# Kernel tuning notes

Hardware: AMD Instinct MI355X
Metric: run time of the kernel (lower is better)

The kernel has to match this reference:

```python
import jax, jax.numpy as jnp
import numpy as np

N, M, D = 2048, 2048, 8


def setup_inputs() -> dict:
    key = jax.random.key(0)
    k1, k2 = jax.random.split(key)
    x = jax.random.normal(k1, (N, D), dtype=jnp.float32)
    xx = jax.random.normal(k2, (M, D), dtype=jnp.float32)
    # free-form params: positive(p) = exp(p); free_form(1.0) = log(1.0) = 0
    scale_free = jnp.zeros((D,), dtype=jnp.float32)
    variance_free = jnp.zeros((), dtype=jnp.float32)
    return {"x": x, "xx": xx, "scale_free": scale_free, "variance_free": variance_free}


def reference(x, xx, scale_free, variance_free):
    # RBF.matrices(x, xx, d_dx=True, d_dxx=True, d_dxdxx=True)
    iscale = 1.0 / jnp.exp(scale_free)            # [D]
    variance = jnp.exp(variance_free)             # scalar, = self.diag()
    r = (x[:, None, :] - xx[None, :, :]) * iscale  # [N,M,D]
    cov = jnp.exp(-0.5 * jnp.sum(r * r, axis=-1)) * variance  # [N,M]
    rr = r * iscale                                # [N,M,D]
    cov_r = cov[..., None] * rr                    # [N,M,D]
    dx = -cov_r                                    # dK/dx
    dxx = cov_r                                    # dK/dxx
    # rirj[..., i, j] = -rr_i * rr_j ; add iscale^2 on the diagonal
    rirj = -rr[..., :, None] * rr[..., None, :] + jnp.diag(iscale * iscale)  # [N,M,D,D]
    dxdxx = rirj * cov[..., None, None]            # d2K/dx dxx
    return (cov, dx, dxx, dxdxx)
```

## Files before the change

kernel.cpp:

```cpp
#include <hip/hip_runtime.h>

#define PN 2048
#define PM 2048
#define PD 8


#define NM_TOT   (PN * PM)
#define BLOCKS_A (NM_TOT * 16 / 256)
#define BLOCKS_B (NM_TOT * 2 / 256)
#define BLOCKS_C (NM_TOT / 256)

__global__ void rbf_precompute(const float* __restrict__ scale_free,
                               const float* __restrict__ var_free,
                               float* __restrict__ ws) {
    const int t = threadIdx.x;
    if (t < PD) {
        const float is = __expf(-scale_free[t]);
        ws[t]     = is;
        ws[9 + t] = is * is;
    }
    if (t == PD) ws[8] = __expf(var_free[0]);
}

__global__ __launch_bounds__(256) void rbf_all_kernel(
    const float* __restrict__ x,
    const float* __restrict__ xx,
    const float* __restrict__ ws,
    float* __restrict__ out)
{
    const unsigned tid = threadIdx.x;
    const unsigned bid = blockIdx.x;

    float is[PD], is2[PD];
#pragma unroll
    for (int d = 0; d < PD; ++d) { is[d] = ws[d]; is2[d] = ws[9 + d]; }
    const float variance = ws[8];

    const size_t NM = (size_t)PN * PM;
    float* covp   = out;
    float* dxp    = out + NM;
    float* dxxp   = out + NM + NM * PD;
    float* dxdxxp = out + NM + 2 * NM * PD;

    auto compute_pair = [&](unsigned p, float r[PD]) -> float {
        const unsigned n = p >> 11;
        const unsigned m = p & 2047u;
        const float4* x4  = reinterpret_cast<const float4*>(x  + (size_t)n * PD);
        const float4* xx4 = reinterpret_cast<const float4*>(xx + (size_t)m * PD);
        const float4 xa = x4[0],  xb = x4[1];
        const float4 ya = xx4[0], yb = xx4[1];
        r[0] = (xa.x - ya.x) * is[0];
        r[1] = (xa.y - ya.y) * is[1];
        r[2] = (xa.z - ya.z) * is[2];
        r[3] = (xa.w - ya.w) * is[3];
        r[4] = (xb.x - yb.x) * is[4];
        r[5] = (xb.y - yb.y) * is[5];
        r[6] = (xb.z - yb.z) * is[6];
        r[7] = (xb.w - yb.w) * is[7];
        float s = 0.f;
#pragma unroll
        for (int d = 0; d < PD; ++d) s += r[d] * r[d];
        return __expf(-0.5f * s) * variance;
    };

    if (bid < BLOCKS_A) {
        const unsigned g = bid * 256u + tid;
        const unsigned p = g >> 4;
        const unsigned i = g & 15u;
        float r[PD];
        const float cov = compute_pair(p, r);
        float rr[PD];
#pragma unroll
        for (int d = 0; d < PD; ++d) rr[d] = r[d] * is[d];

        const unsigned row = i >> 1;
        const unsigned c0  = (i & 1u) * 4u;
        const float a = -cov * rr[row];
        float v[4];
#pragma unroll
        for (int j = 0; j < 4; ++j) v[j] = a * rr[c0 + j];
        if (row >= c0 && row < c0 + 4u) v[row - c0] += cov * is2[row];

        float4* d2 = reinterpret_cast<float4*>(dxdxxp + (size_t)g * 4);
        *d2 = make_float4(v[0], v[1], v[2], v[3]);
    } else if (bid < BLOCKS_A + BLOCKS_B) {
        const unsigned g = (bid - BLOCKS_A) * 256u + tid;
        const unsigned p = g >> 1;
        const unsigned c0 = (g & 1u) * 4u;
        float r[PD];
        const float cov = compute_pair(p, r);
        float w[4];
#pragma unroll
        for (int j = 0; j < 4; ++j) w[j] = cov * r[c0 + j] * is[c0 + j];

        float4* ddx  = reinterpret_cast<float4*>(dxp  + (size_t)g * 4);
        float4* ddxx = reinterpret_cast<float4*>(dxxp + (size_t)g * 4);
        *ddx  = make_float4(-w[0], -w[1], -w[2], -w[3]);
        *ddxx = make_float4( w[0],  w[1],  w[2],  w[3]);
    } else {
        const unsigned p = (bid - BLOCKS_A - BLOCKS_B) * 256u + tid;
        float r[PD];
        covp[p] = compute_pair(p, r);
    }
}

extern "C" void kernel_launch(void* const* d_in, const int* in_sizes, int n_in,
                              void* d_out, int out_size, void* d_ws, size_t ws_size,
                              hipStream_t stream) {
    const float* x  = (const float*)d_in[0];
    const float* xx = (const float*)d_in[1];
    const float* sf = (const float*)d_in[2];
    const float* vf = (const float*)d_in[3];
    float* out = (float*)d_out;
    float* ws  = (float*)d_ws;

    rbf_precompute<<<1, 64, 0, stream>>>(sf, vf, ws);

    const int grid = BLOCKS_A + BLOCKS_B + BLOCKS_C;
    rbf_all_kernel<<<grid, 256, 0, stream>>>(x, xx, ws, out);
}
```

Measured before the change: 1.423 ms.

## Compute each pair once per thread and share via LDS for all outputs

```diff
diff --git a/kernel.cpp b/kernel.cpp
--- a/kernel.cpp
+++ b/kernel.cpp
@@ -4,11 +4,8 @@
 #define PM 2048
 #define PD 8
 
+#define NM ((size_t)PN * (size_t)PM)
 
-#define NM_TOT   (PN * PM)
-#define BLOCKS_A (NM_TOT * 16 / 256)
-#define BLOCKS_B (NM_TOT * 2 / 256)
-#define BLOCKS_C (NM_TOT / 256)
 
 __global__ void rbf_precompute(const float* __restrict__ scale_free,
                                const float* __restrict__ var_free,
@@ -28,79 +25,93 @@
     const float* __restrict__ ws,
     float* __restrict__ out)
 {
+    __shared__ __align__(16) float lds[256 * 12];
+
     const unsigned tid = threadIdx.x;
     const unsigned bid = blockIdx.x;
 
-    float is[PD], is2[PD];
+    float is[PD];
 #pragma unroll
-    for (int d = 0; d < PD; ++d) { is[d] = ws[d]; is2[d] = ws[9 + d]; }
+    for (int d = 0; d < PD; ++d) is[d] = ws[d];
     const float variance = ws[8];
 
-    const size_t NM = (size_t)PN * PM;
     float* covp   = out;
     float* dxp    = out + NM;
     float* dxxp   = out + NM + NM * PD;
     float* dxdxxp = out + NM + 2 * NM * PD;
 
-    auto compute_pair = [&](unsigned p, float r[PD]) -> float {
-        const unsigned n = p >> 11;
-        const unsigned m = p & 2047u;
-        const float4* x4  = reinterpret_cast<const float4*>(x  + (size_t)n * PD);
-        const float4* xx4 = reinterpret_cast<const float4*>(xx + (size_t)m * PD);
-        const float4 xa = x4[0],  xb = x4[1];
-        const float4 ya = xx4[0], yb = xx4[1];
-        r[0] = (xa.x - ya.x) * is[0];
-        r[1] = (xa.y - ya.y) * is[1];
-        r[2] = (xa.z - ya.z) * is[2];
-        r[3] = (xa.w - ya.w) * is[3];
-        r[4] = (xb.x - yb.x) * is[4];
-        r[5] = (xb.y - yb.y) * is[5];
-        r[6] = (xb.z - yb.z) * is[6];
-        r[7] = (xb.w - yb.w) * is[7];
-        float s = 0.f;
+    const unsigned p = bid * 256u + tid;
+    const unsigned n = p >> 11;
+    const unsigned m = p & 2047u;
+    const float4* x4  = reinterpret_cast<const float4*>(x  + (size_t)n * PD);
+    const float4* xx4 = reinterpret_cast<const float4*>(xx + (size_t)m * PD);
+    const float4 xa = x4[0],  xb = x4[1];
+    const float4 ya = xx4[0], yb = xx4[1];
+
+    float r[PD];
+    r[0] = (xa.x - ya.x) * is[0];
+    r[1] = (xa.y - ya.y) * is[1];
+    r[2] = (xa.z - ya.z) * is[2];
+    r[3] = (xa.w - ya.w) * is[3];
+    r[4] = (xb.x - yb.x) * is[4];
+    r[5] = (xb.y - yb.y) * is[5];
+    r[6] = (xb.z - yb.z) * is[6];
+    r[7] = (xb.w - yb.w) * is[7];
+
+    float s = 0.f;
 #pragma unroll
-        for (int d = 0; d < PD; ++d) s += r[d] * r[d];
-        return __expf(-0.5f * s) * variance;
-    };
+    for (int d = 0; d < PD; ++d) s += r[d] * r[d];
+    const float cov = __expf(-0.5f * s) * variance;
 
-    if (bid < BLOCKS_A) {
-        const unsigned g = bid * 256u + tid;
-        const unsigned p = g >> 4;
-        const unsigned i = g & 15u;
-        float r[PD];
-        const float cov = compute_pair(p, r);
-        float rr[PD];
+    float rr[PD];
 #pragma unroll
-        for (int d = 0; d < PD; ++d) rr[d] = r[d] * is[d];
+    for (int d = 0; d < PD; ++d) rr[d] = r[d] * is[d];
 
-        const unsigned row = i >> 1;
-        const unsigned c0  = (i & 1u) * 4u;
-        const float a = -cov * rr[row];
-        float v[4];
+    float4* lrow = reinterpret_cast<float4*>(&lds[tid * 12u]);
+    lrow[0] = make_float4(rr[0], rr[1], rr[2], rr[3]);
+    lrow[1] = make_float4(rr[4], rr[5], rr[6], rr[7]);
+    lds[tid * 12u + 8u] = cov;
+
+    covp[p] = cov;
+
+    __syncthreads();
+
 #pragma unroll
-        for (int j = 0; j < 4; ++j) v[j] = a * rr[c0 + j];
-        if (row >= c0 && row < c0 + 4u) v[row - c0] += cov * is2[row];
+    for (int s2 = 0; s2 < 2; ++s2) {
+        const unsigned c2 = (unsigned)s2 * 256u + tid;
+        const unsigned q  = c2 >> 1;
+        const unsigned c0 = (c2 & 1u) * 4u;
+        const float4 rr4 = *reinterpret_cast<const float4*>(&lds[q * 12u + c0]);
+        const float covq = lds[q * 12u + 8u];
+        const float4 w = make_float4(covq * rr4.x, covq * rr4.y,
+                                     covq * rr4.z, covq * rr4.w);
+        const size_t off = (size_t)bid * 2048u + (size_t)c2 * 4u;
+        *reinterpret_cast<float4*>(dxp  + off) = make_float4(-w.x, -w.y, -w.z, -w.w);
+        *reinterpret_cast<float4*>(dxxp + off) = w;
+    }
 
-        float4* d2 = reinterpret_cast<float4*>(dxdxxp + (size_t)g * 4);
-        *d2 = make_float4(v[0], v[1], v[2], v[3]);
-    } else if (bid < BLOCKS_A + BLOCKS_B) {
-        const unsigned g = (bid - BLOCKS_A) * 256u + tid;
-        const unsigned p = g >> 1;
-        const unsigned c0 = (g & 1u) * 4u;
-        float r[PD];
-        const float cov = compute_pair(p, r);
-        float w[4];
+    const unsigned t15  = tid & 15u;
+    const unsigned row  = t15 >> 1;
+    const unsigned c0d  = (t15 & 1u) * 4u;
+    const int dcol = (int)row - (int)c0d;
+    const float is2row = ws[9u + row];
+    const unsigned qbase = tid >> 4;
+
 #pragma unroll
-        for (int j = 0; j < 4; ++j) w[j] = cov * r[c0 + j] * is[c0 + j];
-
-        float4* ddx  = reinterpret_cast<float4*>(dxp  + (size_t)g * 4);
-        float4* ddxx = reinterpret_cast<float4*>(dxxp + (size_t)g * 4);
-        *ddx  = make_float4(-w[0], -w[1], -w[2], -w[3]);
-        *ddxx = make_float4( w[0],  w[1],  w[2],  w[3]);
-    } else {
-        const unsigned p = (bid - BLOCKS_A - BLOCKS_B) * 256u + tid;
-        float r[PD];
-        covp[p] = compute_pair(p, r);
+    for (int s1 = 0; s1 < 16; ++s1) {
+        const unsigned q = (unsigned)s1 * 16u + qbase;
+        const float4 rr4 = *reinterpret_cast<const float4*>(&lds[q * 12u + c0d]);
+        const float rrow = lds[q * 12u + row];
+        const float covq = lds[q * 12u + 8u];
+        const float a = -covq * rrow;
+        float4 v = make_float4(a * rr4.x, a * rr4.y, a * rr4.z, a * rr4.w);
+        const float dadd = covq * is2row;
+        v.x += (dcol == 0) ? dadd : 0.f;
+        v.y += (dcol == 1) ? dadd : 0.f;
+        v.z += (dcol == 2) ? dadd : 0.f;
+        v.w += (dcol == 3) ? dadd : 0.f;
+        const unsigned c = (unsigned)s1 * 256u + tid;
+        *reinterpret_cast<float4*>(dxdxxp + (size_t)bid * 16384u + (size_t)c * 4u) = v;
     }
 }
 
@@ -116,6 +127,6 @@
 
     rbf_precompute<<<1, 64, 0, stream>>>(sf, vf, ws);
 
-    const int grid = BLOCKS_A + BLOCKS_B + BLOCKS_C;
+    const int grid = (PN * PM) / 256;
     rbf_all_kernel<<<grid, 256, 0, stream>>>(x, xx, ws, out);
 }
```

Result: faster. 1.317 ms (-7.5%).
